# Kernel optimization log

Measured on AMD Instinct MI355X. Metric: run time of the kernel, lower is better.

The kernel has to match this reference:

```python
import jax, jax.numpy as jnp
import numpy as np

B, T, C, H = 2, 2048, 1024, 16
D = C // H  # head dim = 64

def setup_inputs() -> dict:
    key = jax.random.key(0)
    k1, k2, k3 = jax.random.split(key, 3)
    x = jax.random.normal(k1, (B, T, C), dtype=jnp.float32)
    Wqkv = jax.random.normal(k2, (C, 3 * C), dtype=jnp.float32) * (1.0 / np.sqrt(C))
    bqkv = jnp.zeros((3 * C,), dtype=jnp.float32)
    Wproj = jax.random.normal(k3, (C, C), dtype=jnp.float32) * (1.0 / np.sqrt(C))
    bproj = jnp.zeros((C,), dtype=jnp.float32)
    return {"x": x, "Wqkv": Wqkv, "bqkv": bqkv, "Wproj": Wproj, "bproj": bproj}

def reference(x, Wqkv, bqkv, Wproj, bproj):
    b, t, c = x.shape
    qkv = x @ Wqkv + bqkv                      # [B,T,3C]
    q, k, v = jnp.split(qkv, 3, axis=-1)
    # [B,T,C] -> [B,H,T,D]
    def heads(y):
        return y.reshape(b, t, H, D).transpose(0, 2, 1, 3)
    q, k, v = heads(q), heads(k), heads(v)
    scale = 1.0 / np.sqrt(D)
    scores = jnp.einsum('bhqd,bhkd->bhqk', q, k) * scale  # [B,H,T,T]
    causal = jnp.tril(jnp.ones((t, t), dtype=bool))
    scores = jnp.where(causal, scores, jnp.finfo(scores.dtype).min)
    attn = jax.nn.softmax(scores, axis=-1)
    out = jnp.einsum('bhqk,bhkd->bhqd', attn, v)          # [B,H,T,D]
    out = out.transpose(0, 2, 1, 3).reshape(b, t, c)      # [B,T,C]
    return out @ Wproj + bproj
```

## Files before the change

### kernel.cpp

```cpp
#include <hip/hip_runtime.h>
#include <hip/hip_bf16.h>

#define B_ 2
#define T_ 2048
#define C_ 1024
#define H_ 16
#define D_ 64
#define M_ROWS (B_ * T_)
#define N_QKV (3 * C_)
#define QKS (2 * C_)

typedef __bf16 bf16x8 __attribute__((ext_vector_type(8)));
typedef float f32x4 __attribute__((ext_vector_type(4)));

#define SC 0.18033688011112042f

__device__ __forceinline__ void gl_lds16(const __bf16* g, __bf16* l) {
    __builtin_amdgcn_global_load_lds(
        (const __attribute__((address_space(1))) unsigned int*)g,
        (__attribute__((address_space(3))) unsigned int*)l, 16, 0, 0);
}

__global__ __launch_bounds__(256) void conv_bf16(const float* __restrict__ in,
                                                 __bf16* __restrict__ out, int n8)
{
    int i = blockIdx.x * 256 + threadIdx.x;
    if (i >= n8) return;
    const float4* p = (const float4*)(in + (size_t)i * 8);
    float4 a = p[0], b = p[1];
    __bf16 v[8] = {(__bf16)a.x, (__bf16)a.y, (__bf16)a.z, (__bf16)a.w,
                   (__bf16)b.x, (__bf16)b.y, (__bf16)b.z, (__bf16)b.w};
    *(uint4*)(out + (size_t)i * 8) = *(uint4*)v;
}

__global__ __launch_bounds__(256) void transp_w2(
    const float* __restrict__ Wqkv, const float* __restrict__ Wproj,
    __bf16* __restrict__ Wqkvt, __bf16* __restrict__ Wprojt)
{
    __shared__ __bf16 Ts[64 * 72];
    const int tid = threadIdx.x;
    const int gy = blockIdx.y;
    const float* W; __bf16* Wt; int N, n0;
    if (gy < 48) { W = Wqkv;  Wt = Wqkvt;  N = N_QKV; n0 = gy * 64; }
    else         { W = Wproj; Wt = Wprojt; N = C_;    n0 = (gy - 48) * 64; }
    const int k0 = blockIdx.x * 64;
#pragma unroll
    for (int i = 0; i < 4; ++i) {
        int f = i * 256 + tid;
        int r = f >> 4, c4 = (f & 15) * 4;
        float4 v = *(const float4*)(W + (size_t)(k0 + r) * N + n0 + c4);
        Ts[(c4 + 0) * 72 + r] = (__bf16)v.x;
        Ts[(c4 + 1) * 72 + r] = (__bf16)v.y;
        Ts[(c4 + 2) * 72 + r] = (__bf16)v.z;
        Ts[(c4 + 3) * 72 + r] = (__bf16)v.w;
    }
    __syncthreads();
#pragma unroll
    for (int i = 0; i < 2; ++i) {
        int f = i * 256 + tid;
        int n = f >> 3, c8 = (f & 7) * 8;
        *(uint4*)(Wt + (size_t)(n0 + n) * C_ + k0 + c8) = *(const uint4*)&Ts[n * 72 + c8];
    }
}

#define GBK 64

__global__ __launch_bounds__(256) void gemm_qkv(
    const __bf16* __restrict__ A, const __bf16* __restrict__ Bt,
    const float* __restrict__ bias, __bf16* __restrict__ qk,
    __bf16* __restrict__ vt)
{
    __shared__ __bf16 As[128 * GBK];
    __shared__ __bf16 Bs[128 * GBK];

    const int tid  = threadIdx.x;
    const int m0   = blockIdx.x * 128;
    const int n0   = blockIdx.y * 128;
    const int w    = tid >> 6;
    const int lane = tid & 63;
    const int quad = lane >> 4;
    const int l16  = lane & 15;
    const int wr   = (w >> 1) * 64;
    const int wc   = (w & 1) * 64;
    const int K = C_, N = N_QKV;

    const int srow = w * 32 + (lane >> 3);
    const int sseg = ((lane & 7) ^ (lane >> 3)) * 8;
    const __bf16* Ag = A + (size_t)(m0 + srow) * K + sseg;
    const __bf16* Bg = Bt + (size_t)(n0 + srow) * K + sseg;

    f32x4 acc[4][4] = {};

    for (int k0 = 0; k0 < K; k0 += GBK) {
#pragma unroll
        for (int i = 0; i < 4; ++i) {
            gl_lds16(Ag + k0 + (size_t)(i * 8) * K, &As[(w * 32 + i * 8) * GBK]);
            gl_lds16(Bg + k0 + (size_t)(i * 8) * K, &Bs[(w * 32 + i * 8) * GBK]);
        }
        __syncthreads();
#pragma unroll
        for (int kk = 0; kk < 2; ++kk) {
            bf16x8 af[4], bf[4];
#pragma unroll
            for (int mi = 0; mi < 4; ++mi)
                af[mi] = *(const bf16x8*)&As[(wr + mi * 16 + l16) * GBK +
                                             (((kk * 4 + quad) ^ (l16 & 7)) * 8)];
#pragma unroll
            for (int ni = 0; ni < 4; ++ni)
                bf[ni] = *(const bf16x8*)&Bs[(wc + ni * 16 + l16) * GBK +
                                             (((kk * 4 + quad) ^ (l16 & 7)) * 8)];
#pragma unroll
            for (int mi = 0; mi < 4; ++mi)
#pragma unroll
                for (int ni = 0; ni < 4; ++ni)
                    acc[mi][ni] = __builtin_amdgcn_mfma_f32_16x16x32_bf16(
                        af[mi], bf[ni], acc[mi][ni], 0, 0, 0);
        }
        __syncthreads();
    }

    if (n0 < 2 * C_) {
#pragma unroll
        for (int mi = 0; mi < 4; ++mi) {
#pragma unroll
            for (int ni = 0; ni < 4; ++ni) {
                int col = n0 + wc + ni * 16 + l16;
                float bv = bias[col];
#pragma unroll
                for (int r = 0; r < 4; ++r) {
                    int row = m0 + wr + mi * 16 + quad * 4 + r;
                    qk[(size_t)row * QKS + col] = (__bf16)(acc[mi][ni][r] + bv);
                }
            }
        }
    } else {
        const int bb = m0 >> 11;
        const int tb = (m0 & (T_ - 1)) + wr;
#pragma unroll
        for (int mi = 0; mi < 4; ++mi) {
#pragma unroll
            for (int ni = 0; ni < 4; ++ni) {
                int col = n0 + wc + ni * 16 + l16;
                float bv = bias[col];
                int c = col - 2 * C_;
                int t0 = tb + mi * 16 + quad * 4;
                __bf16 pb[4];
#pragma unroll
                for (int r = 0; r < 4; ++r)
                    pb[r] = (__bf16)(acc[mi][ni][r] + bv);
                *(uint2*)&vt[((size_t)bb * C_ + c) * T_ + t0] = *(uint2*)pb;
            }
        }
    }
}

__global__ __launch_bounds__(256) void gemm_proj(
    const __bf16* __restrict__ A, const __bf16* __restrict__ Bt,
    const float* __restrict__ bias, float* __restrict__ C)
{
    __shared__ __bf16 As[128 * GBK];
    __shared__ __bf16 Bs[128 * GBK];

    const int tid  = threadIdx.x;
    const int m0   = blockIdx.x * 128;
    const int n0   = blockIdx.y * 128;
    const int w    = tid >> 6;
    const int lane = tid & 63;
    const int quad = lane >> 4;
    const int l16  = lane & 15;
    const int wr   = (w >> 1) * 64;
    const int wc   = (w & 1) * 64;
    const int K = C_, N = C_;

    const int srow = w * 32 + (lane >> 3);
    const int sseg = ((lane & 7) ^ (lane >> 3)) * 8;
    const __bf16* Ag = A + (size_t)(m0 + srow) * K + sseg;
    const __bf16* Bg = Bt + (size_t)(n0 + srow) * K + sseg;

    f32x4 acc[4][4] = {};

    for (int k0 = 0; k0 < K; k0 += GBK) {
#pragma unroll
        for (int i = 0; i < 4; ++i) {
            gl_lds16(Ag + k0 + (size_t)(i * 8) * K, &As[(w * 32 + i * 8) * GBK]);
            gl_lds16(Bg + k0 + (size_t)(i * 8) * K, &Bs[(w * 32 + i * 8) * GBK]);
        }
        __syncthreads();
#pragma unroll
        for (int kk = 0; kk < 2; ++kk) {
            bf16x8 af[4], bf[4];
#pragma unroll
            for (int mi = 0; mi < 4; ++mi)
                af[mi] = *(const bf16x8*)&As[(wr + mi * 16 + l16) * GBK +
                                             (((kk * 4 + quad) ^ (l16 & 7)) * 8)];
#pragma unroll
            for (int ni = 0; ni < 4; ++ni)
                bf[ni] = *(const bf16x8*)&Bs[(wc + ni * 16 + l16) * GBK +
                                             (((kk * 4 + quad) ^ (l16 & 7)) * 8)];
#pragma unroll
            for (int mi = 0; mi < 4; ++mi)
#pragma unroll
                for (int ni = 0; ni < 4; ++ni)
                    acc[mi][ni] = __builtin_amdgcn_mfma_f32_16x16x32_bf16(
                        af[mi], bf[ni], acc[mi][ni], 0, 0, 0);
        }
        __syncthreads();
    }

#pragma unroll
    for (int mi = 0; mi < 4; ++mi) {
#pragma unroll
        for (int ni = 0; ni < 4; ++ni) {
            int col = n0 + wc + ni * 16 + l16;
            float bv = bias[col];
#pragma unroll
            for (int r = 0; r < 4; ++r) {
                int row = m0 + wr + mi * 16 + quad * 4 + r;
                C[(size_t)row * N + col] = acc[mi][ni][r] + bv;
            }
        }
    }
}

__global__ __launch_bounds__(256) void attn_kernel(
    const __bf16* __restrict__ qk, const __bf16* __restrict__ vt,
    __bf16* __restrict__ out)
{
    __shared__ __bf16 Qs[128 * 64];
    __shared__ __bf16 KVs[4][64 * 64];
    __shared__ __bf16 Ps[4][2][16 * 64];

    const int tid  = threadIdx.x;
    const int bh   = blockIdx.x;
    const int j    = blockIdx.y;
    const int qt   = (j < 8) ? (15 - j) : (j - 8);
    const int b    = bh >> 4;
    const int h    = bh & 15;
    const int w    = tid >> 6;
    const int lane = tid & 63;
    const int quad = lane >> 4;
    const int l16  = lane & 15;
    const int lxor = l16 & 7;

    const int srow = lane >> 3;
    const int sseg = ((lane & 7) ^ srow) * 8;
    const int nkt  = 2 * qt + 2;

    {
        const __bf16* Qg = qk + (size_t)(b * T_ + qt * 128 + w * 32 + srow) * QKS
                         + (size_t)h * 64 + sseg;
#pragma unroll
        for (int i = 0; i < 4; ++i)
            gl_lds16(Qg + (size_t)(i * 8) * QKS, &Qs[(w * 32 + i * 8) * 64]);
        const __bf16* Kg = qk + (size_t)(b * T_ + w * 16 + srow) * QKS
                         + C_ + (size_t)h * 64 + sseg;
        gl_lds16(Kg, &KVs[0][(w * 16) * 64]);
        gl_lds16(Kg + (size_t)8 * QKS, &KVs[0][(w * 16 + 8) * 64]);
        const __bf16* Vg = vt + ((size_t)(b * H_ + h) * 64 + w * 16 + srow) * T_ + sseg;
        gl_lds16(Vg, &KVs[1][(w * 16) * 64]);
        gl_lds16(Vg + (size_t)8 * T_, &KVs[1][(w * 16 + 8) * 64]);
    }
    __syncthreads();

    bf16x8 qf[2][2];
#pragma unroll
    for (int g = 0; g < 2; ++g)
#pragma unroll
        for (int kk = 0; kk < 2; ++kk)
            qf[g][kk] = *(const bf16x8*)&Qs[(g * 64 + w * 16 + l16) * 64 +
                                            (((kk * 4 + quad) ^ lxor) * 8)];

    f32x4 o[2][4] = {};
    float lacc[2] = {0.f, 0.f};

    for (int kt = 0; kt < nkt; ++kt) {
        const __bf16* Ks = KVs[(kt & 1) * 2];
        const __bf16* Vs = KVs[(kt & 1) * 2 + 1];

        if (kt + 1 < nkt) {
            int nb = ((kt + 1) & 1) * 2;
            const __bf16* Kg = qk + (size_t)(b * T_ + (kt + 1) * 64 + w * 16 + srow) * QKS
                             + C_ + (size_t)h * 64 + sseg;
            gl_lds16(Kg, &KVs[nb][(w * 16) * 64]);
            gl_lds16(Kg + (size_t)8 * QKS, &KVs[nb][(w * 16 + 8) * 64]);
            const __bf16* Vg = vt + ((size_t)(b * H_ + h) * 64 + w * 16 + srow) * T_
                             + (kt + 1) * 64 + sseg;
            gl_lds16(Vg, &KVs[nb + 1][(w * 16) * 64]);
            gl_lds16(Vg + (size_t)8 * T_, &KVs[nb + 1][(w * 16 + 8) * 64]);
        }

#pragma unroll
        for (int g = 0; g < 2; ++g) {
            if (g == 0 && kt == nkt - 1) continue;
            f32x4 s[4] = {};
#pragma unroll
            for (int ni = 0; ni < 4; ++ni) {
#pragma unroll
                for (int kk = 0; kk < 2; ++kk) {
                    bf16x8 kf = *(const bf16x8*)&Ks[(ni * 16 + l16) * 64 +
                                                    (((kk * 4 + quad) ^ lxor) * 8)];
                    s[ni] = __builtin_amdgcn_mfma_f32_16x16x32_bf16(kf, qf[g][kk], s[ni], 0, 0, 0);
                }
            }
            if (kt == 2 * qt + g) {
#pragma unroll
                for (int ni = 0; ni < 4; ++ni)
#pragma unroll
                    for (int r = 0; r < 4; ++r)
                        if (ni * 16 + quad * 4 + r > w * 16 + l16) s[ni][r] = -3.0e38f;
            }
            __bf16* Psw = &Ps[w][g][0];
            float la = 0.f;
#pragma unroll
            for (int ni = 0; ni < 4; ++ni) {
                __bf16 pb[4];
#pragma unroll
                for (int r = 0; r < 4; ++r) {
                    float pe = __builtin_amdgcn_exp2f(s[ni][r] * SC);
                    la += pe;
                    pb[r] = (__bf16)pe;
                }
                int seg = (ni * 2 + (quad >> 1)) ^ lxor;
                *(uint2*)&Psw[l16 * 64 + seg * 8 + (quad & 1) * 4] = *(uint2*)pb;
            }
            lacc[g] += la;
        }
        __threadfence_block();

#pragma unroll
        for (int ni = 0; ni < 4; ++ni) {
#pragma unroll
            for (int kk = 0; kk < 2; ++kk) {
                bf16x8 vf = *(const bf16x8*)&Vs[(ni * 16 + l16) * 64 +
                                                (((kk * 4 + quad) ^ lxor) * 8)];
#pragma unroll
                for (int g = 0; g < 2; ++g) {
                    if (g == 0 && kt == nkt - 1) continue;
                    bf16x8 pf = *(const bf16x8*)&Ps[w][g][l16 * 64 +
                                                        (((kk * 4 + quad) ^ lxor) * 8)];
                    o[g][ni] = __builtin_amdgcn_mfma_f32_16x16x32_bf16(pf, vf, o[g][ni], 0, 0, 0);
                }
            }
        }
        __syncthreads();
    }

#pragma unroll
    for (int g = 0; g < 2; ++g) {
        float la = lacc[g];
        la += __shfl_xor(la, 16, 64);
        la += __shfl_xor(la, 32, 64);
#pragma unroll
        for (int r = 0; r < 4; ++r) {
            float linv = 1.f / __shfl(la, quad * 4 + r, 64);
            int trow = qt * 128 + g * 64 + w * 16 + quad * 4 + r;
#pragma unroll
            for (int ni = 0; ni < 4; ++ni)
                out[((size_t)(b * T_ + trow)) * C_ + h * 64 + ni * 16 + l16] =
                    (__bf16)(o[g][ni][r] * linv);
        }
    }
}

extern "C" void kernel_launch(void* const* d_in, const int* in_sizes, int n_in,
                              void* d_out, int out_size, void* d_ws, size_t ws_size,
                              hipStream_t stream)
{
    const float* x     = (const float*)d_in[0];
    const float* Wqkv  = (const float*)d_in[1];
    const float* bqkv  = (const float*)d_in[2];
    const float* Wproj = (const float*)d_in[3];
    const float* bproj = (const float*)d_in[4];
    float* out = (float*)d_out;

    char* ws = (char*)d_ws;
    __bf16* xb     = (__bf16*)(ws);
    __bf16* Wqkvt  = (__bf16*)(ws + (8u  << 20));
    __bf16* Wprojt = (__bf16*)(ws + (14u << 20));
    __bf16* qk     = (__bf16*)(ws + (16u << 20));
    __bf16* vt     = (__bf16*)(ws + (32u << 20));
    __bf16* att    = xb;

    conv_bf16<<<(M_ROWS * C_ / 8 + 255) / 256, 256, 0, stream>>>(x, xb, M_ROWS * C_ / 8);
    transp_w2<<<dim3(16, 64), 256, 0, stream>>>(Wqkv, Wproj, Wqkvt, Wprojt);

    gemm_qkv<<<dim3(M_ROWS / 128, N_QKV / 128), 256, 0, stream>>>(
        xb, Wqkvt, bqkv, qk, vt);

    attn_kernel<<<dim3(32, 16), 256, 0, stream>>>(qk, vt, att);

    gemm_proj<<<dim3(M_ROWS / 128, C_ / 128), 256, 0, stream>>>(
        att, Wprojt, bproj, out);
}
```

Before: 192.1 us.

## Restructure causal attention into paired 64-row query tiles per block

Each attention block now handles two 64-row query tiles, p and 31-p, one after the other, instead of one 128-row tile processed as two groups. Pairing a short tile with a long one evens out causal work across blocks and halves the Q and P shared-memory footprint. The cost is that K/V tiles are no longer shared between two query groups, so K/V traffic and LDS reads per FLOP roughly double. The launch grid must also change to 16 blocks in y, which is in the launcher and not shown here.

```diff
diff --git a/kernel.cpp b/kernel.cpp
--- a/kernel.cpp
+++ b/kernel.cpp
@@ -82,7 +82,7 @@
     const int l16  = lane & 15;
     const int wr   = (w >> 1) * 64;
     const int wc   = (w & 1) * 64;
-    const int K = C_, N = N_QKV;
+    const int K = C_;
 
     const int srow = w * 32 + (lane >> 3);
     const int sseg = ((lane & 7) ^ (lane >> 3)) * 8;
@@ -226,14 +226,13 @@
     const __bf16* __restrict__ qk, const __bf16* __restrict__ vt,
     __bf16* __restrict__ out)
 {
-    __shared__ __bf16 Qs[128 * 64];
+    __shared__ __bf16 Qs[64 * 64];
     __shared__ __bf16 KVs[4][64 * 64];
-    __shared__ __bf16 Ps[4][2][16 * 64];
+    __shared__ __bf16 Ps[4][16 * 64];
 
     const int tid  = threadIdx.x;
     const int bh   = blockIdx.x;
-    const int j    = blockIdx.y;
-    const int qt   = (j < 8) ? (15 - j) : (j - 8);
+    const int p    = blockIdx.y;
     const int b    = bh >> 4;
     const int h    = bh & 15;
     const int w    = tid >> 6;
@@ -244,54 +243,50 @@
 
     const int srow = lane >> 3;
     const int sseg = ((lane & 7) ^ srow) * 8;
-    const int nkt  = 2 * qt + 2;
-
-    {
-        const __bf16* Qg = qk + (size_t)(b * T_ + qt * 128 + w * 32 + srow) * QKS
-                         + (size_t)h * 64 + sseg;
-#pragma unroll
-        for (int i = 0; i < 4; ++i)
-            gl_lds16(Qg + (size_t)(i * 8) * QKS, &Qs[(w * 32 + i * 8) * 64]);
-        const __bf16* Kg = qk + (size_t)(b * T_ + w * 16 + srow) * QKS
-                         + C_ + (size_t)h * 64 + sseg;
-        gl_lds16(Kg, &KVs[0][(w * 16) * 64]);
-        gl_lds16(Kg + (size_t)8 * QKS, &KVs[0][(w * 16 + 8) * 64]);
-        const __bf16* Vg = vt + ((size_t)(b * H_ + h) * 64 + w * 16 + srow) * T_ + sseg;
-        gl_lds16(Vg, &KVs[1][(w * 16) * 64]);
-        gl_lds16(Vg + (size_t)8 * T_, &KVs[1][(w * 16 + 8) * 64]);
-    }
-    __syncthreads();
-
-    bf16x8 qf[2][2];
-#pragma unroll
-    for (int g = 0; g < 2; ++g)
+    __bf16* Psw = &Ps[w][0];
+
+    for (int half = 0; half < 2; ++half) {
+        const int qt = half ? (31 - p) : p;
+
+        {
+            const __bf16* Qg = qk + (size_t)(b * T_ + qt * 64 + w * 16 + srow) * QKS
+                             + (size_t)h * 64 + sseg;
+            gl_lds16(Qg, &Qs[(w * 16) * 64]);
+            gl_lds16(Qg + (size_t)8 * QKS, &Qs[(w * 16 + 8) * 64]);
+            const __bf16* Kg = qk + (size_t)(b * T_ + w * 16 + srow) * QKS
+                             + C_ + (size_t)h * 64 + sseg;
+            gl_lds16(Kg, &KVs[0][(w * 16) * 64]);
+            gl_lds16(Kg + (size_t)8 * QKS, &KVs[0][(w * 16 + 8) * 64]);
+            const __bf16* Vg = vt + ((size_t)(b * H_ + h) * 64 + w * 16 + srow) * T_ + sseg;
+            gl_lds16(Vg, &KVs[1][(w * 16) * 64]);
+            gl_lds16(Vg + (size_t)8 * T_, &KVs[1][(w * 16 + 8) * 64]);
+        }
+        __syncthreads();
+
+        bf16x8 qf[2];
 #pragma unroll
         for (int kk = 0; kk < 2; ++kk)
-            qf[g][kk] = *(const bf16x8*)&Qs[(g * 64 + w * 16 + l16) * 64 +
-                                            (((kk * 4 + quad) ^ lxor) * 8)];
-
-    f32x4 o[2][4] = {};
-    float lacc[2] = {0.f, 0.f};
-
-    for (int kt = 0; kt < nkt; ++kt) {
-        const __bf16* Ks = KVs[(kt & 1) * 2];
-        const __bf16* Vs = KVs[(kt & 1) * 2 + 1];
-
-        if (kt + 1 < nkt) {
-            int nb = ((kt + 1) & 1) * 2;
-            const __bf16* Kg = qk + (size_t)(b * T_ + (kt + 1) * 64 + w * 16 + srow) * QKS
-                             + C_ + (size_t)h * 64 + sseg;
-            gl_lds16(Kg, &KVs[nb][(w * 16) * 64]);
-            gl_lds16(Kg + (size_t)8 * QKS, &KVs[nb][(w * 16 + 8) * 64]);
-            const __bf16* Vg = vt + ((size_t)(b * H_ + h) * 64 + w * 16 + srow) * T_
-                             + (kt + 1) * 64 + sseg;
-            gl_lds16(Vg, &KVs[nb + 1][(w * 16) * 64]);
-            gl_lds16(Vg + (size_t)8 * T_, &KVs[nb + 1][(w * 16 + 8) * 64]);
-        }
-
-#pragma unroll
-        for (int g = 0; g < 2; ++g) {
-            if (g == 0 && kt == nkt - 1) continue;
+            qf[kk] = *(const bf16x8*)&Qs[(w * 16 + l16) * 64 + (((kk * 4 + quad) ^ lxor) * 8)];
+
+        f32x4 o[4] = {};
+        float lacc = 0.f;
+
+        for (int kt = 0; kt <= qt; ++kt) {
+            const __bf16* Ks = KVs[(kt & 1) * 2];
+            const __bf16* Vs = KVs[(kt & 1) * 2 + 1];
+
+            if (kt < qt) {
+                int nb = ((kt + 1) & 1) * 2;
+                const __bf16* Kg = qk + (size_t)(b * T_ + (kt + 1) * 64 + w * 16 + srow) * QKS
+                                 + C_ + (size_t)h * 64 + sseg;
+                gl_lds16(Kg, &KVs[nb][(w * 16) * 64]);
+                gl_lds16(Kg + (size_t)8 * QKS, &KVs[nb][(w * 16 + 8) * 64]);
+                const __bf16* Vg = vt + ((size_t)(b * H_ + h) * 64 + w * 16 + srow) * T_
+                                 + (kt + 1) * 64 + sseg;
+                gl_lds16(Vg, &KVs[nb + 1][(w * 16) * 64]);
+                gl_lds16(Vg + (size_t)8 * T_, &KVs[nb + 1][(w * 16 + 8) * 64]);
+            }
+
             f32x4 s[4] = {};
 #pragma unroll
             for (int ni = 0; ni < 4; ++ni) {
@@ -299,65 +294,59 @@
                 for (int kk = 0; kk < 2; ++kk) {
                     bf16x8 kf = *(const bf16x8*)&Ks[(ni * 16 + l16) * 64 +
                                                     (((kk * 4 + quad) ^ lxor) * 8)];
-                    s[ni] = __builtin_amdgcn_mfma_f32_16x16x32_bf16(kf, qf[g][kk], s[ni], 0, 0, 0);
+                    s[ni] = __builtin_amdgcn_mfma_f32_16x16x32_bf16(kf, qf[kk], s[ni], 0, 0, 0);
                 }
             }
-            if (kt == 2 * qt + g) {
+
+            if (kt == qt) {
 #pragma unroll
                 for (int ni = 0; ni < 4; ++ni)
 #pragma unroll
                     for (int r = 0; r < 4; ++r)
                         if (ni * 16 + quad * 4 + r > w * 16 + l16) s[ni][r] = -3.0e38f;
             }
-            __bf16* Psw = &Ps[w][g][0];
-            float la = 0.f;
+
 #pragma unroll
             for (int ni = 0; ni < 4; ++ni) {
                 __bf16 pb[4];
 #pragma unroll
                 for (int r = 0; r < 4; ++r) {
                     float pe = __builtin_amdgcn_exp2f(s[ni][r] * SC);
-                    la += pe;
+                    lacc += pe;
                     pb[r] = (__bf16)pe;
                 }
                 int seg = (ni * 2 + (quad >> 1)) ^ lxor;
                 *(uint2*)&Psw[l16 * 64 + seg * 8 + (quad & 1) * 4] = *(uint2*)pb;
             }
-            lacc[g] += la;
-        }
-        __threadfence_block();
-
-#pragma unroll
-        for (int ni = 0; ni < 4; ++ni) {
-#pragma unroll
-            for (int kk = 0; kk < 2; ++kk) {
-                bf16x8 vf = *(const bf16x8*)&Vs[(ni * 16 + l16) * 64 +
-                                                (((kk * 4 + quad) ^ lxor) * 8)];
-#pragma unroll
-                for (int g = 0; g < 2; ++g) {
-                    if (g == 0 && kt == nkt - 1) continue;
-                    bf16x8 pf = *(const bf16x8*)&Ps[w][g][l16 * 64 +
-                                                        (((kk * 4 + quad) ^ lxor) * 8)];
-                    o[g][ni] = __builtin_amdgcn_mfma_f32_16x16x32_bf16(pf, vf, o[g][ni], 0, 0, 0);
+            __threadfence_block();
+
+            bf16x8 pf[2];
+#pragma unroll
+            for (int kk = 0; kk < 2; ++kk)
+                pf[kk] = *(const bf16x8*)&Psw[l16 * 64 + (((kk * 4 + quad) ^ lxor) * 8)];
+#pragma unroll
+            for (int ni = 0; ni < 4; ++ni) {
+#pragma unroll
+                for (int kk = 0; kk < 2; ++kk) {
+                    bf16x8 vf = *(const bf16x8*)&Vs[(ni * 16 + l16) * 64 +
+                                                    (((kk * 4 + quad) ^ lxor) * 8)];
+                    o[ni] = __builtin_amdgcn_mfma_f32_16x16x32_bf16(pf[kk], vf, o[ni], 0, 0, 0);
                 }
             }
-        }
-        __syncthreads();
-    }
-
-#pragma unroll
-    for (int g = 0; g < 2; ++g) {
-        float la = lacc[g];
-        la += __shfl_xor(la, 16, 64);
-        la += __shfl_xor(la, 32, 64);
+            __syncthreads();
+        }
+
+        lacc += __shfl_xor(lacc, 16, 64);
+        lacc += __shfl_xor(lacc, 32, 64);
+
 #pragma unroll
         for (int r = 0; r < 4; ++r) {
-            float linv = 1.f / __shfl(la, quad * 4 + r, 64);
-            int trow = qt * 128 + g * 64 + w * 16 + quad * 4 + r;
+            float linv = 1.f / __shfl(lacc, quad * 4 + r, 64);
+            int trow = qt * 64 + w * 16 + quad * 4 + r;
 #pragma unroll
             for (int ni = 0; ni < 4; ++ni)
                 out[((size_t)(b * T_ + trow)) * C_ + h * 64 + ni * 16 + l16] =
-                    (__bf16)(o[g][ni][r] * linv);
+                    (__bf16)(o[ni][r] * linv);
         }
     }
 }
```

Measured after the change: 175.4 us. 8.7% less time.

## Merge prep kernels and pair causal query tiles per attention block

Applied to the files above, without the earlier changes.

Fuses the x fp32-to-bf16 conversion and weight transposes into a single prep launch, removing one kernel launch. The attention grid is halved, and each block now processes two query tiles (p and 15-p) in sequence so every block does the same amount of causal work. This evens out load across blocks and removes tail imbalance, but leaves only 256 blocks, which may underfill the GPU. The two tiles run serially, with no overlap between them.

```diff
diff --git a/kernel.cpp b/kernel.cpp
--- a/kernel.cpp
+++ b/kernel.cpp
@@ -21,29 +21,31 @@
         (__attribute__((address_space(3))) unsigned int*)l, 16, 0, 0);
 }
 
-__global__ __launch_bounds__(256) void conv_bf16(const float* __restrict__ in,
-                                                 __bf16* __restrict__ out, int n8)
-{
-    int i = blockIdx.x * 256 + threadIdx.x;
-    if (i >= n8) return;
-    const float4* p = (const float4*)(in + (size_t)i * 8);
-    float4 a = p[0], b = p[1];
-    __bf16 v[8] = {(__bf16)a.x, (__bf16)a.y, (__bf16)a.z, (__bf16)a.w,
-                   (__bf16)b.x, (__bf16)b.y, (__bf16)b.z, (__bf16)b.w};
-    *(uint4*)(out + (size_t)i * 8) = *(uint4*)v;
-}
-
-__global__ __launch_bounds__(256) void transp_w2(
-    const float* __restrict__ Wqkv, const float* __restrict__ Wproj,
+__global__ __launch_bounds__(256) void prep(
+    const float* __restrict__ x, const float* __restrict__ Wqkv,
+    const float* __restrict__ Wproj, __bf16* __restrict__ xb,
     __bf16* __restrict__ Wqkvt, __bf16* __restrict__ Wprojt)
 {
     __shared__ __bf16 Ts[64 * 72];
     const int tid = threadIdx.x;
-    const int gy = blockIdx.y;
+    int bid = blockIdx.x;
+
+    if (bid < 2048) {
+        int i = bid * 256 + tid;
+        const float4* pp = (const float4*)(x + (size_t)i * 8);
+        float4 a = pp[0], b = pp[1];
+        __bf16 v[8] = {(__bf16)a.x, (__bf16)a.y, (__bf16)a.z, (__bf16)a.w,
+                       (__bf16)b.x, (__bf16)b.y, (__bf16)b.z, (__bf16)b.w};
+        *(uint4*)(xb + (size_t)i * 8) = *(uint4*)v;
+        return;
+    }
+    bid -= 2048;
+    const int kx = bid & 15;
+    const int gy = bid >> 4;
     const float* W; __bf16* Wt; int N, n0;
     if (gy < 48) { W = Wqkv;  Wt = Wqkvt;  N = N_QKV; n0 = gy * 64; }
     else         { W = Wproj; Wt = Wprojt; N = C_;    n0 = (gy - 48) * 64; }
-    const int k0 = blockIdx.x * 64;
+    const int k0 = kx * 64;
 #pragma unroll
     for (int i = 0; i < 4; ++i) {
         int f = i * 256 + tid;
@@ -82,7 +84,7 @@
     const int l16  = lane & 15;
     const int wr   = (w >> 1) * 64;
     const int wc   = (w & 1) * 64;
-    const int K = C_, N = N_QKV;
+    const int K = C_;
 
     const int srow = w * 32 + (lane >> 3);
     const int sseg = ((lane & 7) ^ (lane >> 3)) * 8;
@@ -232,8 +234,7 @@
 
     const int tid  = threadIdx.x;
     const int bh   = blockIdx.x;
-    const int j    = blockIdx.y;
-    const int qt   = (j < 8) ? (15 - j) : (j - 8);
+    const int p    = blockIdx.y;
     const int b    = bh >> 4;
     const int h    = bh & 15;
     const int w    = tid >> 6;
@@ -244,120 +245,124 @@
 
     const int srow = lane >> 3;
     const int sseg = ((lane & 7) ^ srow) * 8;
-    const int nkt  = 2 * qt + 2;
-
-    {
-        const __bf16* Qg = qk + (size_t)(b * T_ + qt * 128 + w * 32 + srow) * QKS
-                         + (size_t)h * 64 + sseg;
-#pragma unroll
-        for (int i = 0; i < 4; ++i)
-            gl_lds16(Qg + (size_t)(i * 8) * QKS, &Qs[(w * 32 + i * 8) * 64]);
-        const __bf16* Kg = qk + (size_t)(b * T_ + w * 16 + srow) * QKS
-                         + C_ + (size_t)h * 64 + sseg;
-        gl_lds16(Kg, &KVs[0][(w * 16) * 64]);
-        gl_lds16(Kg + (size_t)8 * QKS, &KVs[0][(w * 16 + 8) * 64]);
-        const __bf16* Vg = vt + ((size_t)(b * H_ + h) * 64 + w * 16 + srow) * T_ + sseg;
-        gl_lds16(Vg, &KVs[1][(w * 16) * 64]);
-        gl_lds16(Vg + (size_t)8 * T_, &KVs[1][(w * 16 + 8) * 64]);
-    }
-    __syncthreads();
-
-    bf16x8 qf[2][2];
-#pragma unroll
-    for (int g = 0; g < 2; ++g)
-#pragma unroll
-        for (int kk = 0; kk < 2; ++kk)
-            qf[g][kk] = *(const bf16x8*)&Qs[(g * 64 + w * 16 + l16) * 64 +
-                                            (((kk * 4 + quad) ^ lxor) * 8)];
-
-    f32x4 o[2][4] = {};
-    float lacc[2] = {0.f, 0.f};
-
-    for (int kt = 0; kt < nkt; ++kt) {
-        const __bf16* Ks = KVs[(kt & 1) * 2];
-        const __bf16* Vs = KVs[(kt & 1) * 2 + 1];
-
-        if (kt + 1 < nkt) {
-            int nb = ((kt + 1) & 1) * 2;
-            const __bf16* Kg = qk + (size_t)(b * T_ + (kt + 1) * 64 + w * 16 + srow) * QKS
+
+    for (int half = 0; half < 2; ++half) {
+        const int qt  = half ? (15 - p) : p;
+        const int nkt = 2 * qt + 2;
+
+        {
+            const __bf16* Qg = qk + (size_t)(b * T_ + qt * 128 + w * 32 + srow) * QKS
+                             + (size_t)h * 64 + sseg;
+#pragma unroll
+            for (int i = 0; i < 4; ++i)
+                gl_lds16(Qg + (size_t)(i * 8) * QKS, &Qs[(w * 32 + i * 8) * 64]);
+            const __bf16* Kg = qk + (size_t)(b * T_ + w * 16 + srow) * QKS
                              + C_ + (size_t)h * 64 + sseg;
-            gl_lds16(Kg, &KVs[nb][(w * 16) * 64]);
-            gl_lds16(Kg + (size_t)8 * QKS, &KVs[nb][(w * 16 + 8) * 64]);
-            const __bf16* Vg = vt + ((size_t)(b * H_ + h) * 64 + w * 16 + srow) * T_
-                             + (kt + 1) * 64 + sseg;
-            gl_lds16(Vg, &KVs[nb + 1][(w * 16) * 64]);
-            gl_lds16(Vg + (size_t)8 * T_, &KVs[nb + 1][(w * 16 + 8) * 64]);
+            gl_lds16(Kg, &KVs[0][(w * 16) * 64]);
+            gl_lds16(Kg + (size_t)8 * QKS, &KVs[0][(w * 16 + 8) * 64]);
+            const __bf16* Vg = vt + ((size_t)(b * H_ + h) * 64 + w * 16 + srow) * T_ + sseg;
+            gl_lds16(Vg, &KVs[1][(w * 16) * 64]);
+            gl_lds16(Vg + (size_t)8 * T_, &KVs[1][(w * 16 + 8) * 64]);
+        }
+        __syncthreads();
+
+        bf16x8 qf[2][2];
+#pragma unroll
+        for (int g = 0; g < 2; ++g)
+#pragma unroll
+            for (int kk = 0; kk < 2; ++kk)
+                qf[g][kk] = *(const bf16x8*)&Qs[(g * 64 + w * 16 + l16) * 64 +
+                                                (((kk * 4 + quad) ^ lxor) * 8)];
+
+        f32x4 o[2][4] = {};
+        float lacc[2] = {0.f, 0.f};
+
+        for (int kt = 0; kt < nkt; ++kt) {
+            const __bf16* Ks = KVs[(kt & 1) * 2];
+            const __bf16* Vs = KVs[(kt & 1) * 2 + 1];
+
+            if (kt + 1 < nkt) {
+                int nb = ((kt + 1) & 1) * 2;
+                const __bf16* Kg = qk + (size_t)(b * T_ + (kt + 1) * 64 + w * 16 + srow) * QKS
+                                 + C_ + (size_t)h * 64 + sseg;
+                gl_lds16(Kg, &KVs[nb][(w * 16) * 64]);
+                gl_lds16(Kg + (size_t)8 * QKS, &KVs[nb][(w * 16 + 8) * 64]);
+                const __bf16* Vg = vt + ((size_t)(b * H_ + h) * 64 + w * 16 + srow) * T_
+                                 + (kt + 1) * 64 + sseg;
+                gl_lds16(Vg, &KVs[nb + 1][(w * 16) * 64]);
+                gl_lds16(Vg + (size_t)8 * T_, &KVs[nb + 1][(w * 16 + 8) * 64]);
+            }
+
+#pragma unroll
+            for (int g = 0; g < 2; ++g) {
+                if (g == 0 && kt == nkt - 1) continue;
+                f32x4 s[4] = {};
+#pragma unroll
+                for (int ni = 0; ni < 4; ++ni) {
+#pragma unroll
+                    for (int kk = 0; kk < 2; ++kk) {
+                        bf16x8 kf = *(const bf16x8*)&Ks[(ni * 16 + l16) * 64 +
+                                                        (((kk * 4 + quad) ^ lxor) * 8)];
+                        s[ni] = __builtin_amdgcn_mfma_f32_16x16x32_bf16(kf, qf[g][kk], s[ni], 0, 0, 0);
+                    }
+                }
+                if (kt == 2 * qt + g) {
+#pragma unroll
+                    for (int ni = 0; ni < 4; ++ni)
+#pragma unroll
+                        for (int r = 0; r < 4; ++r)
+                            if (ni * 16 + quad * 4 + r > w * 16 + l16) s[ni][r] = -3.0e38f;
+                }
+                __bf16* Psw = &Ps[w][g][0];
+                float la = 0.f;
+#pragma unroll
+                for (int ni = 0; ni < 4; ++ni) {
+                    __bf16 pb[4];
+#pragma unroll
+                    for (int r = 0; r < 4; ++r) {
+                        float pe = __builtin_amdgcn_exp2f(s[ni][r] * SC);
+                        la += pe;
+                        pb[r] = (__bf16)pe;
+                    }
+                    int seg = (ni * 2 + (quad >> 1)) ^ lxor;
+                    *(uint2*)&Psw[l16 * 64 + seg * 8 + (quad & 1) * 4] = *(uint2*)pb;
+                }
+                lacc[g] += la;
+            }
+            __threadfence_block();
+
+#pragma unroll
+            for (int ni = 0; ni < 4; ++ni) {
+#pragma unroll
+                for (int kk = 0; kk < 2; ++kk) {
+                    bf16x8 vf = *(const bf16x8*)&Vs[(ni * 16 + l16) * 64 +
+                                                    (((kk * 4 + quad) ^ lxor) * 8)];
+#pragma unroll
+                    for (int g = 0; g < 2; ++g) {
+                        if (g == 0 && kt == nkt - 1) continue;
+                        bf16x8 pf = *(const bf16x8*)&Ps[w][g][l16 * 64 +
+                                                            (((kk * 4 + quad) ^ lxor) * 8)];
+                        o[g][ni] = __builtin_amdgcn_mfma_f32_16x16x32_bf16(pf, vf, o[g][ni], 0, 0, 0);
+                    }
+                }
+            }
+            __syncthreads();
         }
 
 #pragma unroll
         for (int g = 0; g < 2; ++g) {
-            if (g == 0 && kt == nkt - 1) continue;
-            f32x4 s[4] = {};
-#pragma unroll
-            for (int ni = 0; ni < 4; ++ni) {
-#pragma unroll
-                for (int kk = 0; kk < 2; ++kk) {
-                    bf16x8 kf = *(const bf16x8*)&Ks[(ni * 16 + l16) * 64 +
-                                                    (((kk * 4 + quad) ^ lxor) * 8)];
-                    s[ni] = __builtin_amdgcn_mfma_f32_16x16x32_bf16(kf, qf[g][kk], s[ni], 0, 0, 0);
-                }
-            }
-            if (kt == 2 * qt + g) {
+            float la = lacc[g];
+            la += __shfl_xor(la, 16, 64);
+            la += __shfl_xor(la, 32, 64);
+#pragma unroll
+            for (int r = 0; r < 4; ++r) {
+                float linv = 1.f / __shfl(la, quad * 4 + r, 64);
+                int trow = qt * 128 + g * 64 + w * 16 + quad * 4 + r;
 #pragma unroll
                 for (int ni = 0; ni < 4; ++ni)
-#pragma unroll
-                    for (int r = 0; r < 4; ++r)
-                        if (ni * 16 + quad * 4 + r > w * 16 + l16) s[ni][r] = -3.0e38f;
-            }
-            __bf16* Psw = &Ps[w][g][0];
-            float la = 0.f;
-#pragma unroll
-            for (int ni = 0; ni < 4; ++ni) {
-                __bf16 pb[4];
-#pragma unroll
-                for (int r = 0; r < 4; ++r) {
-                    float pe = __builtin_amdgcn_exp2f(s[ni][r] * SC);
-                    la += pe;
-                    pb[r] = (__bf16)pe;
-                }
-                int seg = (ni * 2 + (quad >> 1)) ^ lxor;
-                *(uint2*)&Psw[l16 * 64 + seg * 8 + (quad & 1) * 4] = *(uint2*)pb;
-            }
-            lacc[g] += la;
-        }
-        __threadfence_block();
-
-#pragma unroll
-        for (int ni = 0; ni < 4; ++ni) {
-#pragma unroll
-            for (int kk = 0; kk < 2; ++kk) {
-                bf16x8 vf = *(const bf16x8*)&Vs[(ni * 16 + l16) * 64 +
-                                                (((kk * 4 + quad) ^ lxor) * 8)];
-#pragma unroll
-                for (int g = 0; g < 2; ++g) {
-                    if (g == 0 && kt == nkt - 1) continue;
-                    bf16x8 pf = *(const bf16x8*)&Ps[w][g][l16 * 64 +
-                                                        (((kk * 4 + quad) ^ lxor) * 8)];
-                    o[g][ni] = __builtin_amdgcn_mfma_f32_16x16x32_bf16(pf, vf, o[g][ni], 0, 0, 0);
-                }
-            }
-        }
-        __syncthreads();
-    }
-
-#pragma unroll
-    for (int g = 0; g < 2; ++g) {
-        float la = lacc[g];
-        la += __shfl_xor(la, 16, 64);
-        la += __shfl_xor(la, 32, 64);
-#pragma unroll
-        for (int r = 0; r < 4; ++r) {
-            float linv = 1.f / __shfl(la, quad * 4 + r, 64);
-            int trow = qt * 128 + g * 64 + w * 16 + quad * 4 + r;
-#pragma unroll
-            for (int ni = 0; ni < 4; ++ni)
-                out[((size_t)(b * T_ + trow)) * C_ + h * 64 + ni * 16 + l16] =
-                    (__bf16)(o[g][ni][r] * linv);
+                    out[((size_t)(b * T_ + trow)) * C_ + h * 64 + ni * 16 + l16] =
+                        (__bf16)(o[g][ni][r] * linv);
+            }
         }
     }
 }
@@ -381,13 +386,12 @@
     __bf16* vt     = (__bf16*)(ws + (32u << 20));
     __bf16* att    = xb;
 
-    conv_bf16<<<(M_ROWS * C_ / 8 + 255) / 256, 256, 0, stream>>>(x, xb, M_ROWS * C_ / 8);
-    transp_w2<<<dim3(16, 64), 256, 0, stream>>>(Wqkv, Wproj, Wqkvt, Wprojt);
+    prep<<<3072, 256, 0, stream>>>(x, Wqkv, Wproj, xb, Wqkvt, Wprojt);
 
     gemm_qkv<<<dim3(M_ROWS / 128, N_QKV / 128), 256, 0, stream>>>(
         xb, Wqkvt, bqkv, qk, vt);
 
-    attn_kernel<<<dim3(32, 16), 256, 0, stream>>>(qk, vt, att);
+    attn_kernel<<<dim3(32, 8), 256, 0, stream>>>(qk, vt, att);
 
     gemm_proj<<<dim3(M_ROWS / 128, C_ / 128), 256, 0, stream>>>(
         att, Wprojt, bproj, out);
```

Result: no change. 192.8 us (+0.4%).
